# Kernel tuning notes

Measured on AMD Instinct MI355X. Metric: run time of the kernel, lower is better.

The kernel has to match this reference:

```python
import jax, jax.numpy as jnp
import numpy as np
import math

D_HEAD = 64
EPS = 1e-6


def _rms_norm(x, scale, eps):
    # compute in float32 like the torch reference (promote_types with float32)
    xf = x.astype(jnp.float32)
    ms = jnp.mean(xf * xf, axis=-1, keepdims=True)
    return (xf * (scale.astype(jnp.float32) * jax.lax.rsqrt(ms + eps))).astype(x.dtype)


def _apply_rotary(x, cos, sin):
    # rotate first 2*cos_dim channels, pass the rest through
    ro = cos.shape[-1] * 2
    xr, xp = x[..., :ro], x[..., ro:]
    c = jnp.concatenate([cos, cos], axis=-1)
    s = jnp.concatenate([sin, sin], axis=-1)
    x1, x2 = jnp.split(xr, 2, axis=-1)
    rot = jnp.concatenate([-x2, x1], axis=-1)
    return jnp.concatenate([xr * c + rot * s, xp], axis=-1)


def _nb_idx(L, k):
    # NATTEN neighborhood start: window of size k clamped inside [0, L)
    i = jnp.arange(L)
    start = jnp.clip(i - k // 2, 0, L - k)
    return start[:, None] + jnp.arange(k)[None, :]  # [L, k]


def setup_inputs() -> dict:
    key = jax.random.key(0)
    ks = jax.random.split(key, 6)
    n, H, W, d_model, cond_features = 2, 48, 48, 256, 256
    x = jax.random.normal(ks[0], (n, H, W, d_model), dtype=jnp.float32)
    axis = jnp.linspace(-1.0, 1.0, H, dtype=jnp.float32)
    gh, gw = jnp.meshgrid(axis, axis, indexing='ij')
    pos = jnp.stack([gh, gw], axis=-1)  # [H, W, 2]
    cond = jax.random.normal(ks[1], (n, cond_features), dtype=jnp.float32)
    w_norm = jax.random.normal(ks[2], (d_model, cond_features), dtype=jnp.float32) * 0.01
    w_qkv = jax.random.normal(ks[3], (3 * d_model, d_model), dtype=jnp.float32) / math.sqrt(d_model)
    w_out = jax.random.normal(ks[4], (d_model, d_model), dtype=jnp.float32) * 0.02
    return {"x": x, "pos": pos, "cond": cond, "w_norm": w_norm, "w_qkv": w_qkv,
            "w_out": w_out, "kernel_size": 7}


def reference(x, pos, cond, w_norm, w_qkv, w_out, kernel_size):
    n, H, W, d_model = x.shape
    e = D_HEAD
    nh = d_model // e
    k = kernel_size
    skip = x

    # AdaRMSNorm: scale = linear(cond) + 1, broadcast over h, w
    scale = (cond @ w_norm.T)[:, None, None, :] + 1.0  # [n,1,1,d_model]
    xn = _rms_norm(x, scale, EPS)

    # QKV projection -> [3, n, nh, H, W, e]
    qkv = (xn @ w_qkv.T).reshape(n, H, W, 3, nh, e)
    qkv = jnp.transpose(qkv, (3, 0, 4, 1, 2, 5))
    q, kk, v = qkv[0], qkv[1], qkv[2]

    # Axial RoPE: freqs buffer of AxialRoPE(d_head // 2)
    dim = e // 2
    nf = dim // 4
    freqs = jnp.exp(jnp.linspace(math.log(math.pi), math.log(10.0 * math.pi), nf + 1)[:-1]).astype(jnp.float32)
    fh = pos[..., 0:1] * freqs  # [H,W,nf]
    fw = pos[..., 1:2] * freqs
    fr = jnp.concatenate([fh, fw], axis=-1)  # [H,W,2*nf] == [H,W,e//4]
    cos, sin = jnp.cos(fr), jnp.sin(fr)
    q = _apply_rotary(q, cos, sin)
    kk = _apply_rotary(kk, cos, sin)
    q = q / math.sqrt(e)

    # 2D neighborhood attention (natten2dqk / natten2dav, dilation 1)
    idx_h = _nb_idx(H, k)  # [H,k]
    idx_w = _nb_idx(W, k)  # [W,k]
    kg = kk[:, :, idx_h][:, :, :, :, idx_w]  # [n,nh,H,k,W,k,e]
    vg = v[:, :, idx_h][:, :, :, :, idx_w]   # [n,nh,H,k,W,k,e]
    qk = jnp.einsum('bmije,bmipjqe->bmijpq', q, kg).reshape(n, nh, H, W, k * k)
    a = jax.nn.softmax(qk, axis=-1).reshape(n, nh, H, W, k, k)
    o = jnp.einsum('bmijpq,bmipjqe->bmije', a, vg)  # [n,nh,H,W,e]

    o = jnp.transpose(o, (0, 2, 3, 1, 4)).reshape(n, H, W, d_model)
    return o @ w_out.T + skip
```

## Files before the change

kernel.cpp:

```cpp
#include <hip/hip_runtime.h>
#include <math.h>

#define N_B 2
#define HH 48
#define WW 48
#define DM 256
#define NH 4
#define EH 64
#define KS 7
#define NPIX (N_B*HH*WW)

typedef _Float16 half8 __attribute__((ext_vector_type(8)));
typedef float float4v __attribute__((ext_vector_type(4)));

__global__ void scale_kernel(const float* __restrict__ cond,
                             const float* __restrict__ w_norm,
                             float* __restrict__ scale) {
    int b = blockIdx.x;
    int t = threadIdx.x, wave = t >> 6, lane = t & 63;
    int d = blockIdx.y*32 + wave*8 + (lane >> 3);
    int l8 = lane & 7;
    const float4* wr4 = (const float4*)(w_norm + (size_t)d*DM) + l8*8;
    const float4* c4  = (const float4*)(cond + (size_t)b*DM) + l8*8;
    float acc = 0.f;
    #pragma unroll
    for (int j = 0; j < 8; ++j) {
        float4 w = wr4[j], c = c4[j];
        acc += w.x*c.x + w.y*c.y + w.z*c.z + w.w*c.w;
    }
    acc += __shfl_xor(acc, 1, 64);
    acc += __shfl_xor(acc, 2, 64);
    acc += __shfl_xor(acc, 4, 64);
    if (l8 == 0) scale[b*DM + d] = acc + 1.0f;
}

__global__ void rmsnorm_kernel(const float* __restrict__ x,
                               const float* __restrict__ scale,
                               _Float16* __restrict__ xn) {
    int pix = blockIdx.x, t = threadIdx.x;
    int b = pix / (HH*WW);
    float v = x[(size_t)pix*DM + t];
    float ss = v*v;
    #pragma unroll
    for (int off = 32; off > 0; off >>= 1) ss += __shfl_xor(ss, off, 64);
    __shared__ float wsum[4];
    if ((t & 63) == 0) wsum[t>>6] = ss;
    __syncthreads();
    float tot = wsum[0]+wsum[1]+wsum[2]+wsum[3];
    float r = rsqrtf(tot*(1.0f/DM) + 1e-6f);
    xn[(size_t)pix*DM + t] = (_Float16)(v * scale[b*DM + t] * r);
}

__global__ __launch_bounds__(256) void gemm_qkv_f16(const _Float16* __restrict__ A,
                                                    const float* __restrict__ B,
                                                    const float* __restrict__ pos,
                                                    _Float16* __restrict__ qh,
                                                    _Float16* __restrict__ kh,
                                                    _Float16* __restrict__ vh) {
    const int K = DM, LDT = 40;
    __shared__ _Float16 As[64*LDT];
    __shared__ _Float16 Bs[64*LDT];
    int t = threadIdx.x;
    int wave = t >> 6, lane = t & 63;
    int m0 = blockIdx.x*64, n0 = blockIdx.y*64;
    int lr = t >> 2, lk = (t & 3) * 8;

    float4v acc[4];
    #pragma unroll
    for (int ni = 0; ni < 4; ++ni) acc[ni] = (float4v){0.f,0.f,0.f,0.f};

    int frow = lane & 15, kq = (lane >> 4) * 8;

    for (int k0 = 0; k0 < K; k0 += 32) {
        half8 a0 = *(const half8*)(A + (size_t)(m0 + lr)*K + k0 + lk);
        const float* bp = B + (size_t)(n0 + lr)*K + k0 + lk;
        float4 b0 = *(const float4*)bp;
        float4 b1 = *(const float4*)(bp + 4);
        half8 hb;
        hb[0]=(_Float16)b0.x; hb[1]=(_Float16)b0.y; hb[2]=(_Float16)b0.z; hb[3]=(_Float16)b0.w;
        hb[4]=(_Float16)b1.x; hb[5]=(_Float16)b1.y; hb[6]=(_Float16)b1.z; hb[7]=(_Float16)b1.w;
        __syncthreads();
        *(half8*)&As[lr*LDT + lk] = a0;
        *(half8*)&Bs[lr*LDT + lk] = hb;
        __syncthreads();
        half8 af = *(const half8*)&As[(wave*16 + frow)*LDT + kq];
        #pragma unroll
        for (int ni = 0; ni < 4; ++ni) {
            half8 bf = *(const half8*)&Bs[(ni*16 + frow)*LDT + kq];
            acc[ni] = __builtin_amdgcn_mfma_f32_16x16x32_f16(af, bf, acc[ni], 0, 0, 0);
        }
    }

    int sel  = n0 >> 8;
    int head = (n0 >> 6) & 3;
    _Float16* outp = (sel == 0) ? qh : (sel == 1) ? kh : vh;
    int col = lane & 15, rbase = (lane >> 4) * 4;
    float freq = __expf(1.14472988585f + (float)(col & 7) * 0.287823136624f);
    #pragma unroll
    for (int r = 0; r < 4; ++r) {
        int pix = m0 + wave*16 + rbase + r;
        float v0 = acc[0][r], v1 = acc[1][r], v2 = acc[2][r], v3 = acc[3][r];
        if (sel < 2) {
            int hw = pix % (HH*WW);
            float p = (col < 8) ? pos[hw*2] : pos[hw*2+1];
            float sn, cs;
            __sincosf(p*freq, &sn, &cs);
            float o0 = v0*cs - v1*sn;
            float o1 = v1*cs + v0*sn;
            v0 = o0; v1 = o1;
            if (sel == 0) { v0*=0.125f; v1*=0.125f; v2*=0.125f; v3*=0.125f; }
        }
        size_t base = (size_t)pix*DM + head*EH;
        outp[base +  0 + col] = (_Float16)v0;
        outp[base + 16 + col] = (_Float16)v1;
        outp[base + 32 + col] = (_Float16)v2;
        outp[base + 48 + col] = (_Float16)v3;
    }
}

__global__ __launch_bounds__(256) void attn_mfma(const _Float16* __restrict__ qg,
                                                 const _Float16* __restrict__ kg,
                                                 const _Float16* __restrict__ vg,
                                                 _Float16* __restrict__ obuf) {
    __shared__ _Float16 VT[64*232];
    __shared__ _Float16 SP[64*232];
    int t = threadIdx.x;
    int wave = t >> 6, lane = t & 63;
    int col = lane & 15, quad = lane >> 4;
    int ty = blockIdx.x / 6, tx = blockIdx.x % 6;
    int b = blockIdx.y >> 2, head = blockIdx.y & 3;
    int qh0 = ty*8, qw0 = tx*8;
    int rh0 = min(max(qh0-3, 0), HH-14);
    int rw0 = min(max(qw0-3, 0), WW-14);

    {
        int nbl = t & 31;
        int e0  = (t >> 5) * 8;
        #pragma unroll
        for (int pass = 0; pass < 7; ++pass) {
            int nb = pass*32 + nbl;
            int nr = nb >> 4, nc = nb & 15;
            int pix = (b*HH + rh0+nr)*WW + rw0 + nc;
            half8 vv = *(const half8*)(vg + (size_t)pix*DM + head*EH + e0);
            #pragma unroll
            for (int i = 0; i < 8; ++i)
                VT[(e0+i)*232 + nb] = vv[i];
        }
    }

    int qidx_a = wave*16 + col;
    int pixq = (b*HH + qh0 + (qidx_a>>3))*WW + qw0 + (qidx_a & 7);
    const _Float16* qp = qg + (size_t)pixq*DM + head*EH;
    half8 qf0 = *(const half8*)(qp + quad*8);
    half8 qf1 = *(const half8*)(qp + 32 + quad*8);

    float4v s[14];
    #pragma unroll
    for (int nr = 0; nr < 14; ++nr) {
        int pixk = (b*HH + rh0+nr)*WW + rw0 + col;
        const _Float16* kp = kg + (size_t)pixk*DM + head*EH;
        half8 kf0 = *(const half8*)(kp + quad*8);
        half8 kf1 = *(const half8*)(kp + 32 + quad*8);
        float4v a = (float4v){0.f,0.f,0.f,0.f};
        a = __builtin_amdgcn_mfma_f32_16x16x32_f16(qf0, kf0, a, 0, 0, 0);
        a = __builtin_amdgcn_mfma_f32_16x16x32_f16(qf1, kf1, a, 0, 0, 0);
        s[nr] = a;
    }

    int sh_[4], uw_[4];
    #pragma unroll
    for (int r = 0; r < 4; ++r) {
        int qidx = wave*16 + quad*4 + r;
        int qhh = qh0 + (qidx>>3), qww = qw0 + (qidx & 7);
        sh_[r] = min(max(qhh-3, 0), HH-KS);
        int sw_ = min(max(qww-3, 0), WW-KS);
        uw_[r] = rw0 + col - sw_;
    }
    #pragma unroll
    for (int nr = 0; nr < 14; ++nr)
        #pragma unroll
        for (int r = 0; r < 4; ++r) {
            int uh = rh0 + nr - sh_[r];
            bool ok = ((unsigned)uh < 7u) && ((unsigned)uw_[r] < 7u);
            s[nr][r] = ok ? s[nr][r] : -1e30f;
        }
    #pragma unroll
    for (int r = 0; r < 4; ++r) {
        float m = s[0][r];
        #pragma unroll
        for (int nr = 1; nr < 14; ++nr) m = fmaxf(m, s[nr][r]);
        m = fmaxf(m, __shfl_xor(m, 1, 64));
        m = fmaxf(m, __shfl_xor(m, 2, 64));
        m = fmaxf(m, __shfl_xor(m, 4, 64));
        m = fmaxf(m, __shfl_xor(m, 8, 64));
        float sum = 0.f;
        #pragma unroll
        for (int nr = 0; nr < 14; ++nr) { float p = __expf(s[nr][r] - m); s[nr][r] = p; sum += p; }
        sum += __shfl_xor(sum, 1, 64);
        sum += __shfl_xor(sum, 2, 64);
        sum += __shfl_xor(sum, 4, 64);
        sum += __shfl_xor(sum, 8, 64);
        float rs = 1.f / sum;
        #pragma unroll
        for (int nr = 0; nr < 14; ++nr)
            SP[(wave*16 + quad*4 + r)*232 + nr*16 + col] = (_Float16)(s[nr][r] * rs);
    }
    __syncthreads();

    float4v o[4];
    #pragma unroll
    for (int dt = 0; dt < 4; ++dt) o[dt] = (float4v){0.f,0.f,0.f,0.f};
    #pragma unroll
    for (int ks = 0; ks < 7; ++ks) {
        half8 pa = *(const half8*)&SP[(wave*16 + col)*232 + ks*32 + quad*8];
        #pragma unroll
        for (int dt = 0; dt < 4; ++dt) {
            half8 vf = *(const half8*)&VT[(dt*16 + col)*232 + ks*32 + quad*8];
            o[dt] = __builtin_amdgcn_mfma_f32_16x16x32_f16(pa, vf, o[dt], 0, 0, 0);
        }
    }
    #pragma unroll
    for (int r = 0; r < 4; ++r) {
        int qidx = wave*16 + quad*4 + r;
        int pix = (b*HH + qh0 + (qidx>>3))*WW + qw0 + (qidx & 7);
        #pragma unroll
        for (int dt = 0; dt < 4; ++dt)
            obuf[(size_t)pix*DM + head*EH + dt*16 + col] = (_Float16)o[dt][r];
    }
}

__global__ __launch_bounds__(256) void gemm_out_f16(const _Float16* __restrict__ A,
                                                    const float* __restrict__ B,
                                                    float* __restrict__ C,
                                                    const float* __restrict__ skip) {
    const int K = DM, N = DM, LDT = 40;
    __shared__ _Float16 As[64*LDT];
    __shared__ _Float16 Bs[64*LDT];
    int t = threadIdx.x;
    int wave = t >> 6, lane = t & 63;
    int m0 = blockIdx.x*64, n0 = blockIdx.y*64;
    int lr = t >> 2, lk = (t & 3) * 8;

    float4v acc[4];
    #pragma unroll
    for (int ni = 0; ni < 4; ++ni) acc[ni] = (float4v){0.f,0.f,0.f,0.f};

    int frow = lane & 15, kq = (lane >> 4) * 8;

    for (int k0 = 0; k0 < K; k0 += 32) {
        half8 a0 = *(const half8*)(A + (size_t)(m0 + lr)*K + k0 + lk);
        const float* bp = B + (size_t)(n0 + lr)*K + k0 + lk;
        float4 b0 = *(const float4*)bp;
        float4 b1 = *(const float4*)(bp + 4);
        half8 hb;
        hb[0]=(_Float16)b0.x; hb[1]=(_Float16)b0.y; hb[2]=(_Float16)b0.z; hb[3]=(_Float16)b0.w;
        hb[4]=(_Float16)b1.x; hb[5]=(_Float16)b1.y; hb[6]=(_Float16)b1.z; hb[7]=(_Float16)b1.w;
        __syncthreads();
        *(half8*)&As[lr*LDT + lk] = a0;
        *(half8*)&Bs[lr*LDT + lk] = hb;
        __syncthreads();
        half8 af = *(const half8*)&As[(wave*16 + frow)*LDT + kq];
        #pragma unroll
        for (int ni = 0; ni < 4; ++ni) {
            half8 bf = *(const half8*)&Bs[(ni*16 + frow)*LDT + kq];
            acc[ni] = __builtin_amdgcn_mfma_f32_16x16x32_f16(af, bf, acc[ni], 0, 0, 0);
        }
    }

    int col = lane & 15, rbase = (lane >> 4) * 4;
    #pragma unroll
    for (int ni = 0; ni < 4; ++ni) {
        #pragma unroll
        for (int r = 0; r < 4; ++r) {
            int row = m0 + wave*16 + rbase + r;
            int c   = n0 + ni*16 + col;
            C[(size_t)row*N + c] = acc[ni][r] + skip[(size_t)row*N + c];
        }
    }
}

extern "C" void kernel_launch(void* const* d_in, const int* in_sizes, int n_in,
                              void* d_out, int out_size, void* d_ws, size_t ws_size,
                              hipStream_t stream) {
    const float* x      = (const float*)d_in[0];
    const float* pos    = (const float*)d_in[1];
    const float* cond   = (const float*)d_in[2];
    const float* w_norm = (const float*)d_in[3];
    const float* w_qkv  = (const float*)d_in[4];
    const float* w_out  = (const float*)d_in[5];
    float* out = (float*)d_out;
    char* base = (char*)d_ws;

    const size_t SZH = (size_t)NPIX*DM*2;
    const size_t PAD = 4096;
    float*    scale  = (float*)(base);
    _Float16* xn_h   = (_Float16*)(base + PAD);
    _Float16* qh     = (_Float16*)(base + PAD + 1*(SZH+PAD));
    _Float16* kh     = (_Float16*)(base + PAD + 2*(SZH+PAD));
    _Float16* vh     = (_Float16*)(base + PAD + 3*(SZH+PAD));
    _Float16* obuf_h = (_Float16*)(base + PAD + 4*(SZH+PAD));

    scale_kernel<<<dim3(N_B, 8), 256, 0, stream>>>(cond, w_norm, scale);
    rmsnorm_kernel<<<dim3(NPIX), dim3(DM), 0, stream>>>(x, scale, xn_h);
    gemm_qkv_f16<<<dim3(NPIX/64, 12), 256, 0, stream>>>(xn_h, w_qkv, pos, qh, kh, vh);
    attn_mfma<<<dim3(36, N_B*NH), 256, 0, stream>>>(qh, kh, vh, obuf_h);
    gemm_out_f16<<<dim3(NPIX/64, DM/64), 256, 0, stream>>>(obuf_h, w_out, out, x);
}
```

Before: 105.8 us.

## Fuse RMSNorm into QKV GEMM, stage full-K tiles, shrink output GEMM tile

Drops the separate RMSNorm kernel. Each QKV GEMM block now loads its 64 rows of x in fp32, computes the per-row RMS with shuffles, applies scale and converts to fp16 straight into shared memory. Both GEMMs now stage the entire K=256 tile once instead of looping over 32-wide slices with two barriers per step. The output GEMM uses 32-row tiles to double the block count. The cost is much larger LDS use per block (about 66KB for QKV), which may lower occupancy. The normalization is also recomputed by each of the 12 column blocks, so x is reread 12 times.

```diff
diff --git a/kernel.cpp b/kernel.cpp
--- a/kernel.cpp
+++ b/kernel.cpp
@@ -34,59 +34,73 @@
     if (l8 == 0) scale[b*DM + d] = acc + 1.0f;
 }
 
-__global__ void rmsnorm_kernel(const float* __restrict__ x,
-                               const float* __restrict__ scale,
-                               _Float16* __restrict__ xn) {
-    int pix = blockIdx.x, t = threadIdx.x;
-    int b = pix / (HH*WW);
-    float v = x[(size_t)pix*DM + t];
-    float ss = v*v;
-    #pragma unroll
-    for (int off = 32; off > 0; off >>= 1) ss += __shfl_xor(ss, off, 64);
-    __shared__ float wsum[4];
-    if ((t & 63) == 0) wsum[t>>6] = ss;
-    __syncthreads();
-    float tot = wsum[0]+wsum[1]+wsum[2]+wsum[3];
-    float r = rsqrtf(tot*(1.0f/DM) + 1e-6f);
-    xn[(size_t)pix*DM + t] = (_Float16)(v * scale[b*DM + t] * r);
-}
-
-__global__ __launch_bounds__(256) void gemm_qkv_f16(const _Float16* __restrict__ A,
-                                                    const float* __restrict__ B,
-                                                    const float* __restrict__ pos,
-                                                    _Float16* __restrict__ qh,
-                                                    _Float16* __restrict__ kh,
-                                                    _Float16* __restrict__ vh) {
-    const int K = DM, LDT = 40;
-    __shared__ _Float16 As[64*LDT];
-    __shared__ _Float16 Bs[64*LDT];
+__global__ __launch_bounds__(256) void fused_qkv(const float* __restrict__ x,
+                                                 const float* __restrict__ scale,
+                                                 const float* __restrict__ B,
+                                                 const float* __restrict__ pos,
+                                                 _Float16* __restrict__ qh,
+                                                 _Float16* __restrict__ kh,
+                                                 _Float16* __restrict__ vh) {
+    const int K = DM, LDA = 264;
+    __shared__ _Float16 As[64*LDA];
+    __shared__ _Float16 Bs[64*LDA];
+    __shared__ float scale_sh[DM];
     int t = threadIdx.x;
     int wave = t >> 6, lane = t & 63;
     int m0 = blockIdx.x*64, n0 = blockIdx.y*64;
-    int lr = t >> 2, lk = (t & 3) * 8;
-
+    int b = m0 / (HH*WW);
+
+    scale_sh[t] = scale[b*DM + t];
+
+    int row = t >> 2, seg = t & 3;
+    const float4* xp = (const float4*)(x + (size_t)(m0+row)*DM + seg*64);
+    float4 xr[16];
+    float ss = 0.f;
+    #pragma unroll
+    for (int j = 0; j < 16; ++j) {
+        xr[j] = xp[j];
+        ss += xr[j].x*xr[j].x + xr[j].y*xr[j].y + xr[j].z*xr[j].z + xr[j].w*xr[j].w;
+    }
+    ss += __shfl_xor(ss, 1, 64);
+    ss += __shfl_xor(ss, 2, 64);
+    float rms = rsqrtf(ss*(1.0f/DM) + 1e-6f);
+    __syncthreads();
+
+    #pragma unroll
+    for (int j = 0; j < 8; ++j) {
+        int ch = seg*64 + j*8;
+        float4 a = xr[2*j], c = xr[2*j+1];
+        half8 hv;
+        hv[0]=(_Float16)(a.x*scale_sh[ch+0]*rms); hv[1]=(_Float16)(a.y*scale_sh[ch+1]*rms);
+        hv[2]=(_Float16)(a.z*scale_sh[ch+2]*rms); hv[3]=(_Float16)(a.w*scale_sh[ch+3]*rms);
+        hv[4]=(_Float16)(c.x*scale_sh[ch+4]*rms); hv[5]=(_Float16)(c.y*scale_sh[ch+5]*rms);
+        hv[6]=(_Float16)(c.z*scale_sh[ch+6]*rms); hv[7]=(_Float16)(c.w*scale_sh[ch+7]*rms);
+        *(half8*)&As[row*LDA + ch] = hv;
+    }
+    {
+        const float4* bp = (const float4*)(B + (size_t)(n0+row)*K + seg*64);
+        #pragma unroll
+        for (int j = 0; j < 8; ++j) {
+            float4 b0 = bp[2*j], b1 = bp[2*j+1];
+            half8 hb;
+            hb[0]=(_Float16)b0.x; hb[1]=(_Float16)b0.y; hb[2]=(_Float16)b0.z; hb[3]=(_Float16)b0.w;
+            hb[4]=(_Float16)b1.x; hb[5]=(_Float16)b1.y; hb[6]=(_Float16)b1.z; hb[7]=(_Float16)b1.w;
+            *(half8*)&Bs[row*LDA + seg*64 + j*8] = hb;
+        }
+    }
+    __syncthreads();
+
+    int frow = lane & 15, kq = (lane >> 4) * 8;
     float4v acc[4];
     #pragma unroll
     for (int ni = 0; ni < 4; ++ni) acc[ni] = (float4v){0.f,0.f,0.f,0.f};
-
-    int frow = lane & 15, kq = (lane >> 4) * 8;
-
-    for (int k0 = 0; k0 < K; k0 += 32) {
-        half8 a0 = *(const half8*)(A + (size_t)(m0 + lr)*K + k0 + lk);
-        const float* bp = B + (size_t)(n0 + lr)*K + k0 + lk;
-        float4 b0 = *(const float4*)bp;
-        float4 b1 = *(const float4*)(bp + 4);
-        half8 hb;
-        hb[0]=(_Float16)b0.x; hb[1]=(_Float16)b0.y; hb[2]=(_Float16)b0.z; hb[3]=(_Float16)b0.w;
-        hb[4]=(_Float16)b1.x; hb[5]=(_Float16)b1.y; hb[6]=(_Float16)b1.z; hb[7]=(_Float16)b1.w;
-        __syncthreads();
-        *(half8*)&As[lr*LDT + lk] = a0;
-        *(half8*)&Bs[lr*LDT + lk] = hb;
-        __syncthreads();
-        half8 af = *(const half8*)&As[(wave*16 + frow)*LDT + kq];
+    #pragma unroll
+    for (int ks = 0; ks < 8; ++ks) {
+        int k0 = ks*32;
+        half8 af = *(const half8*)&As[(wave*16 + frow)*LDA + k0 + kq];
         #pragma unroll
         for (int ni = 0; ni < 4; ++ni) {
-            half8 bf = *(const half8*)&Bs[(ni*16 + frow)*LDT + kq];
+            half8 bf = *(const half8*)&Bs[(ni*16 + frow)*LDA + k0 + kq];
             acc[ni] = __builtin_amdgcn_mfma_f32_16x16x32_f16(af, bf, acc[ni], 0, 0, 0);
         }
     }
@@ -233,48 +247,59 @@
                                                     const float* __restrict__ B,
                                                     float* __restrict__ C,
                                                     const float* __restrict__ skip) {
-    const int K = DM, N = DM, LDT = 40;
-    __shared__ _Float16 As[64*LDT];
-    __shared__ _Float16 Bs[64*LDT];
+    const int K = DM, N = DM, LDA = 264;
+    __shared__ _Float16 As[32*LDA];
+    __shared__ _Float16 Bs[64*LDA];
     int t = threadIdx.x;
     int wave = t >> 6, lane = t & 63;
-    int m0 = blockIdx.x*64, n0 = blockIdx.y*64;
-    int lr = t >> 2, lk = (t & 3) * 8;
-
-    float4v acc[4];
-    #pragma unroll
-    for (int ni = 0; ni < 4; ++ni) acc[ni] = (float4v){0.f,0.f,0.f,0.f};
+    int m0 = blockIdx.x*32, n0 = blockIdx.y*64;
+
+    {
+        int row = t >> 3, seg = t & 7;
+        const _Float16* ap = A + (size_t)(m0+row)*K + seg*32;
+        #pragma unroll
+        for (int j = 0; j < 4; ++j)
+            *(half8*)&As[row*LDA + seg*32 + j*8] = *(const half8*)(ap + j*8);
+    }
+    {
+        int row = t >> 2, seg = t & 3;
+        const float4* bp = (const float4*)(B + (size_t)(n0+row)*K + seg*64);
+        #pragma unroll
+        for (int j = 0; j < 8; ++j) {
+            float4 b0 = bp[2*j], b1 = bp[2*j+1];
+            half8 hb;
+            hb[0]=(_Float16)b0.x; hb[1]=(_Float16)b0.y; hb[2]=(_Float16)b0.z; hb[3]=(_Float16)b0.w;
+            hb[4]=(_Float16)b1.x; hb[5]=(_Float16)b1.y; hb[6]=(_Float16)b1.z; hb[7]=(_Float16)b1.w;
+            *(half8*)&Bs[row*LDA + seg*64 + j*8] = hb;
+        }
+    }
+    __syncthreads();
 
     int frow = lane & 15, kq = (lane >> 4) * 8;
-
-    for (int k0 = 0; k0 < K; k0 += 32) {
-        half8 a0 = *(const half8*)(A + (size_t)(m0 + lr)*K + k0 + lk);
-        const float* bp = B + (size_t)(n0 + lr)*K + k0 + lk;
-        float4 b0 = *(const float4*)bp;
-        float4 b1 = *(const float4*)(bp + 4);
-        half8 hb;
-        hb[0]=(_Float16)b0.x; hb[1]=(_Float16)b0.y; hb[2]=(_Float16)b0.z; hb[3]=(_Float16)b0.w;
-        hb[4]=(_Float16)b1.x; hb[5]=(_Float16)b1.y; hb[6]=(_Float16)b1.z; hb[7]=(_Float16)b1.w;
-        __syncthreads();
-        *(half8*)&As[lr*LDT + lk] = a0;
-        *(half8*)&Bs[lr*LDT + lk] = hb;
-        __syncthreads();
-        half8 af = *(const half8*)&As[(wave*16 + frow)*LDT + kq];
-        #pragma unroll
-        for (int ni = 0; ni < 4; ++ni) {
-            half8 bf = *(const half8*)&Bs[(ni*16 + frow)*LDT + kq];
+    int mrow  = (wave & 1) * 16;
+    int nbase = (wave >> 1) * 32;
+    float4v acc[2];
+    acc[0] = (float4v){0.f,0.f,0.f,0.f};
+    acc[1] = (float4v){0.f,0.f,0.f,0.f};
+    #pragma unroll
+    for (int ks = 0; ks < 8; ++ks) {
+        int k0 = ks*32;
+        half8 af = *(const half8*)&As[(mrow + frow)*LDA + k0 + kq];
+        #pragma unroll
+        for (int ni = 0; ni < 2; ++ni) {
+            half8 bf = *(const half8*)&Bs[(nbase + ni*16 + frow)*LDA + k0 + kq];
             acc[ni] = __builtin_amdgcn_mfma_f32_16x16x32_f16(af, bf, acc[ni], 0, 0, 0);
         }
     }
 
     int col = lane & 15, rbase = (lane >> 4) * 4;
     #pragma unroll
-    for (int ni = 0; ni < 4; ++ni) {
+    for (int ni = 0; ni < 2; ++ni) {
         #pragma unroll
         for (int r = 0; r < 4; ++r) {
-            int row = m0 + wave*16 + rbase + r;
-            int c   = n0 + ni*16 + col;
-            C[(size_t)row*N + c] = acc[ni][r] + skip[(size_t)row*N + c];
+            int rowg = m0 + mrow + rbase + r;
+            int c    = n0 + nbase + ni*16 + col;
+            C[(size_t)rowg*N + c] = acc[ni][r] + skip[(size_t)rowg*N + c];
         }
     }
 }
@@ -294,15 +319,13 @@
     const size_t SZH = (size_t)NPIX*DM*2;
     const size_t PAD = 4096;
     float*    scale  = (float*)(base);
-    _Float16* xn_h   = (_Float16*)(base + PAD);
-    _Float16* qh     = (_Float16*)(base + PAD + 1*(SZH+PAD));
-    _Float16* kh     = (_Float16*)(base + PAD + 2*(SZH+PAD));
-    _Float16* vh     = (_Float16*)(base + PAD + 3*(SZH+PAD));
-    _Float16* obuf_h = (_Float16*)(base + PAD + 4*(SZH+PAD));
+    _Float16* qh     = (_Float16*)(base + PAD + 0*(SZH+PAD));
+    _Float16* kh     = (_Float16*)(base + PAD + 1*(SZH+PAD));
+    _Float16* vh     = (_Float16*)(base + PAD + 2*(SZH+PAD));
+    _Float16* obuf_h = (_Float16*)(base + PAD + 3*(SZH+PAD));
 
     scale_kernel<<<dim3(N_B, 8), 256, 0, stream>>>(cond, w_norm, scale);
-    rmsnorm_kernel<<<dim3(NPIX), dim3(DM), 0, stream>>>(x, scale, xn_h);
-    gemm_qkv_f16<<<dim3(NPIX/64, 12), 256, 0, stream>>>(xn_h, w_qkv, pos, qh, kh, vh);
+    fused_qkv<<<dim3(NPIX/64, 12), 256, 0, stream>>>(x, scale, w_qkv, pos, qh, kh, vh);
     attn_mfma<<<dim3(36, N_B*NH), 256, 0, stream>>>(qh, kh, vh, obuf_h);
-    gemm_out_f16<<<dim3(NPIX/64, DM/64), 256, 0, stream>>>(obuf_h, w_out, out, x);
-}
+    gemm_out_f16<<<dim3(NPIX/32, DM/64), 256, 0, stream>>>(obuf_h, w_out, out, x);
+}
```

Result: slower. 116.1 us (+9.8%).

## Fuse all five kernels into one persistent megakernel with grid barriers

Applied to the files above, without the earlier changes.

Replaces the five separate launches (scale, rmsnorm, QKV GEMM, neighborhood attention, output GEMM) with a single persistent kernel of 512 blocks. Each stage runs as a grid-stride loop over its tiles, and stages are separated by atomic-counter grid barriers. The intent is to remove per-launch overhead and inter-kernel gaps. In exchange it adds a memset launch, spin-wait barrier costs, and a deadlock risk if all 512 blocks cannot be co-resident. The attention stage has only 288 tiles, so many blocks sit idle there.

```diff
diff --git a/kernel.cpp b/kernel.cpp
--- a/kernel.cpp
+++ b/kernel.cpp
@@ -9,272 +9,287 @@
 #define EH 64
 #define KS 7
 #define NPIX (N_B*HH*WW)
+#define GRID 512
 
 typedef _Float16 half8 __attribute__((ext_vector_type(8)));
 typedef float float4v __attribute__((ext_vector_type(4)));
 
-__global__ void scale_kernel(const float* __restrict__ cond,
-                             const float* __restrict__ w_norm,
-                             float* __restrict__ scale) {
-    int b = blockIdx.x;
-    int t = threadIdx.x, wave = t >> 6, lane = t & 63;
-    int d = blockIdx.y*32 + wave*8 + (lane >> 3);
-    int l8 = lane & 7;
-    const float4* wr4 = (const float4*)(w_norm + (size_t)d*DM) + l8*8;
-    const float4* c4  = (const float4*)(cond + (size_t)b*DM) + l8*8;
-    float acc = 0.f;
-    #pragma unroll
-    for (int j = 0; j < 8; ++j) {
-        float4 w = wr4[j], c = c4[j];
-        acc += w.x*c.x + w.y*c.y + w.z*c.z + w.w*c.w;
-    }
-    acc += __shfl_xor(acc, 1, 64);
-    acc += __shfl_xor(acc, 2, 64);
-    acc += __shfl_xor(acc, 4, 64);
-    if (l8 == 0) scale[b*DM + d] = acc + 1.0f;
-}
-
-__global__ void rmsnorm_kernel(const float* __restrict__ x,
-                               const float* __restrict__ scale,
-                               _Float16* __restrict__ xn) {
-    int pix = blockIdx.x, t = threadIdx.x;
-    int b = pix / (HH*WW);
-    float v = x[(size_t)pix*DM + t];
-    float ss = v*v;
-    #pragma unroll
-    for (int off = 32; off > 0; off >>= 1) ss += __shfl_xor(ss, off, 64);
-    __shared__ float wsum[4];
-    if ((t & 63) == 0) wsum[t>>6] = ss;
-    __syncthreads();
-    float tot = wsum[0]+wsum[1]+wsum[2]+wsum[3];
-    float r = rsqrtf(tot*(1.0f/DM) + 1e-6f);
-    xn[(size_t)pix*DM + t] = (_Float16)(v * scale[b*DM + t] * r);
-}
-
-__global__ __launch_bounds__(256) void gemm_qkv_f16(const _Float16* __restrict__ A,
-                                                    const float* __restrict__ B,
-                                                    const float* __restrict__ pos,
-                                                    _Float16* __restrict__ qh,
-                                                    _Float16* __restrict__ kh,
-                                                    _Float16* __restrict__ vh) {
-    const int K = DM, LDT = 40;
-    __shared__ _Float16 As[64*LDT];
-    __shared__ _Float16 Bs[64*LDT];
+#define GBAR(idx) do { \
+    __syncthreads(); \
+    if (t == 0) { \
+        __threadfence(); \
+        __hip_atomic_fetch_add(&cnt[idx], 1, __ATOMIC_RELEASE, __HIP_MEMORY_SCOPE_AGENT); \
+        while (__hip_atomic_load(&cnt[idx], __ATOMIC_ACQUIRE, __HIP_MEMORY_SCOPE_AGENT) < (int)gridDim.x) \
+            __builtin_amdgcn_s_sleep(1); \
+        __threadfence(); \
+    } \
+    __syncthreads(); \
+} while (0)
+
+__global__ __launch_bounds__(256, 2) void mega(const float* __restrict__ x,
+                                               const float* __restrict__ pos,
+                                               const float* __restrict__ cond,
+                                               const float* __restrict__ w_norm,
+                                               const float* __restrict__ w_qkv,
+                                               const float* __restrict__ w_out,
+                                               float* __restrict__ out,
+                                               int* __restrict__ cnt,
+                                               float* __restrict__ scale,
+                                               _Float16* __restrict__ xn,
+                                               _Float16* __restrict__ qh,
+                                               _Float16* __restrict__ kh,
+                                               _Float16* __restrict__ vh,
+                                               _Float16* __restrict__ obuf) {
+    int bid = blockIdx.x, nblk = gridDim.x;
     int t = threadIdx.x;
     int wave = t >> 6, lane = t & 63;
-    int m0 = blockIdx.x*64, n0 = blockIdx.y*64;
-    int lr = t >> 2, lk = (t & 3) * 8;
-
-    float4v acc[4];
-    #pragma unroll
-    for (int ni = 0; ni < 4; ++ni) acc[ni] = (float4v){0.f,0.f,0.f,0.f};
-
-    int frow = lane & 15, kq = (lane >> 4) * 8;
-
-    for (int k0 = 0; k0 < K; k0 += 32) {
-        half8 a0 = *(const half8*)(A + (size_t)(m0 + lr)*K + k0 + lk);
-        const float* bp = B + (size_t)(n0 + lr)*K + k0 + lk;
-        float4 b0 = *(const float4*)bp;
-        float4 b1 = *(const float4*)(bp + 4);
-        half8 hb;
-        hb[0]=(_Float16)b0.x; hb[1]=(_Float16)b0.y; hb[2]=(_Float16)b0.z; hb[3]=(_Float16)b0.w;
-        hb[4]=(_Float16)b1.x; hb[5]=(_Float16)b1.y; hb[6]=(_Float16)b1.z; hb[7]=(_Float16)b1.w;
+
+    __shared__ union {
+        struct { _Float16 As[64*40]; _Float16 Bs[64*40]; } g;
+        struct { _Float16 VT[64*232]; _Float16 SP[64*232]; } at;
+        float wsum[4];
+    } sm;
+
+    if (bid < 16) {
+        int b = bid & 1, yg = bid >> 1;
+        int d = yg*32 + wave*8 + (lane >> 3);
+        int l8 = lane & 7;
+        const float4* wr4 = (const float4*)(w_norm + (size_t)d*DM) + l8*8;
+        const float4* c4  = (const float4*)(cond + (size_t)b*DM) + l8*8;
+        float acc = 0.f;
+        #pragma unroll
+        for (int j = 0; j < 8; ++j) {
+            float4 w = wr4[j], c = c4[j];
+            acc += w.x*c.x + w.y*c.y + w.z*c.z + w.w*c.w;
+        }
+        acc += __shfl_xor(acc, 1, 64);
+        acc += __shfl_xor(acc, 2, 64);
+        acc += __shfl_xor(acc, 4, 64);
+        if (l8 == 0) scale[b*DM + d] = acc + 1.0f;
+    }
+    GBAR(0);
+
+    for (int pix = bid; pix < NPIX; pix += nblk) {
+        int b = pix / (HH*WW);
+        float v = x[(size_t)pix*DM + t];
+        float ss = v*v;
+        #pragma unroll
+        for (int off = 32; off > 0; off >>= 1) ss += __shfl_xor(ss, off, 64);
+        if ((t & 63) == 0) sm.wsum[t>>6] = ss;
         __syncthreads();
-        *(half8*)&As[lr*LDT + lk] = a0;
-        *(half8*)&Bs[lr*LDT + lk] = hb;
+        float tot = sm.wsum[0]+sm.wsum[1]+sm.wsum[2]+sm.wsum[3];
+        float r = rsqrtf(tot*(1.0f/DM) + 1e-6f);
+        xn[(size_t)pix*DM + t] = (_Float16)(v * scale[b*DM + t] * r);
         __syncthreads();
-        half8 af = *(const half8*)&As[(wave*16 + frow)*LDT + kq];
-        #pragma unroll
-        for (int ni = 0; ni < 4; ++ni) {
-            half8 bf = *(const half8*)&Bs[(ni*16 + frow)*LDT + kq];
-            acc[ni] = __builtin_amdgcn_mfma_f32_16x16x32_f16(af, bf, acc[ni], 0, 0, 0);
+    }
+    GBAR(1);
+
+    {
+        const int K = DM, LDT = 40;
+        int lr = t >> 2, lk = (t & 3) * 8;
+        int frow = lane & 15, kq = (lane >> 4) * 8;
+        int col = lane & 15, rbase = (lane >> 4) * 4;
+        float freq = __expf(1.14472988585f + (float)(col & 7) * 0.287823136624f);
+        for (int tile = bid; tile < 72*12; tile += nblk) {
+            int m0 = (tile % 72)*64, n0 = (tile / 72)*64;
+            float4v acc[4];
+            #pragma unroll
+            for (int ni = 0; ni < 4; ++ni) acc[ni] = (float4v){0.f,0.f,0.f,0.f};
+            for (int k0 = 0; k0 < K; k0 += 32) {
+                half8 a0 = *(const half8*)(xn + (size_t)(m0 + lr)*K + k0 + lk);
+                const float* bp = w_qkv + (size_t)(n0 + lr)*K + k0 + lk;
+                float4 b0 = *(const float4*)bp;
+                float4 b1 = *(const float4*)(bp + 4);
+                half8 hb;
+                hb[0]=(_Float16)b0.x; hb[1]=(_Float16)b0.y; hb[2]=(_Float16)b0.z; hb[3]=(_Float16)b0.w;
+                hb[4]=(_Float16)b1.x; hb[5]=(_Float16)b1.y; hb[6]=(_Float16)b1.z; hb[7]=(_Float16)b1.w;
+                __syncthreads();
+                *(half8*)&sm.g.As[lr*LDT + lk] = a0;
+                *(half8*)&sm.g.Bs[lr*LDT + lk] = hb;
+                __syncthreads();
+                half8 af = *(const half8*)&sm.g.As[(wave*16 + frow)*LDT + kq];
+                #pragma unroll
+                for (int ni = 0; ni < 4; ++ni) {
+                    half8 bf = *(const half8*)&sm.g.Bs[(ni*16 + frow)*LDT + kq];
+                    acc[ni] = __builtin_amdgcn_mfma_f32_16x16x32_f16(af, bf, acc[ni], 0, 0, 0);
+                }
+            }
+            int sel  = n0 >> 8;
+            int head = (n0 >> 6) & 3;
+            _Float16* outp = (sel == 0) ? qh : (sel == 1) ? kh : vh;
+            #pragma unroll
+            for (int r = 0; r < 4; ++r) {
+                int pix = m0 + wave*16 + rbase + r;
+                float v0 = acc[0][r], v1 = acc[1][r], v2 = acc[2][r], v3 = acc[3][r];
+                if (sel < 2) {
+                    int hw = pix % (HH*WW);
+                    float p = (col < 8) ? pos[hw*2] : pos[hw*2+1];
+                    float sn, cs;
+                    __sincosf(p*freq, &sn, &cs);
+                    float o0 = v0*cs - v1*sn;
+                    float o1 = v1*cs + v0*sn;
+                    v0 = o0; v1 = o1;
+                    if (sel == 0) { v0*=0.125f; v1*=0.125f; v2*=0.125f; v3*=0.125f; }
+                }
+                size_t base = (size_t)pix*DM + head*EH;
+                outp[base +  0 + col] = (_Float16)v0;
+                outp[base + 16 + col] = (_Float16)v1;
+                outp[base + 32 + col] = (_Float16)v2;
+                outp[base + 48 + col] = (_Float16)v3;
+            }
+            __syncthreads();
         }
     }
-
-    int sel  = n0 >> 8;
-    int head = (n0 >> 6) & 3;
-    _Float16* outp = (sel == 0) ? qh : (sel == 1) ? kh : vh;
-    int col = lane & 15, rbase = (lane >> 4) * 4;
-    float freq = __expf(1.14472988585f + (float)(col & 7) * 0.287823136624f);
-    #pragma unroll
-    for (int r = 0; r < 4; ++r) {
-        int pix = m0 + wave*16 + rbase + r;
-        float v0 = acc[0][r], v1 = acc[1][r], v2 = acc[2][r], v3 = acc[3][r];
-        if (sel < 2) {
-            int hw = pix % (HH*WW);
-            float p = (col < 8) ? pos[hw*2] : pos[hw*2+1];
-            float sn, cs;
-            __sincosf(p*freq, &sn, &cs);
-            float o0 = v0*cs - v1*sn;
-            float o1 = v1*cs + v0*sn;
-            v0 = o0; v1 = o1;
-            if (sel == 0) { v0*=0.125f; v1*=0.125f; v2*=0.125f; v3*=0.125f; }
+    GBAR(2);
+
+    {
+        int col = lane & 15, quad = lane >> 4;
+        for (int tile = bid; tile < 36*N_B*NH; tile += nblk) {
+            int bx = tile % 36, by = tile / 36;
+            int ty = bx / 6, tx = bx % 6;
+            int b = by >> 2, head = by & 3;
+            int qh0 = ty*8, qw0 = tx*8;
+            int rh0 = min(max(qh0-3, 0), HH-14);
+            int rw0 = min(max(qw0-3, 0), WW-14);
+
+            {
+                int nbl = t & 31;
+                int e0  = (t >> 5) * 8;
+                #pragma unroll
+                for (int pass = 0; pass < 7; ++pass) {
+                    int nb = pass*32 + nbl;
+                    int nr = nb >> 4, nc = nb & 15;
+                    int pix = (b*HH + rh0+nr)*WW + rw0 + nc;
+                    half8 vv = *(const half8*)(vh + (size_t)pix*DM + head*EH + e0);
+                    #pragma unroll
+                    for (int i = 0; i < 8; ++i)
+                        sm.at.VT[(e0+i)*232 + nb] = vv[i];
+                }
+            }
+
+            int qidx_a = wave*16 + col;
+            int pixq = (b*HH + qh0 + (qidx_a>>3))*WW + qw0 + (qidx_a & 7);
+            const _Float16* qp = qh + (size_t)pixq*DM + head*EH;
+            half8 qf0 = *(const half8*)(qp + quad*8);
+            half8 qf1 = *(const half8*)(qp + 32 + quad*8);
+
+            float4v s[14];
+            #pragma unroll
+            for (int nr = 0; nr < 14; ++nr) {
+                int pixk = (b*HH + rh0+nr)*WW + rw0 + col;
+                const _Float16* kp = kh + (size_t)pixk*DM + head*EH;
+                half8 kf0 = *(const half8*)(kp + quad*8);
+                half8 kf1 = *(const half8*)(kp + 32 + quad*8);
+                float4v a = (float4v){0.f,0.f,0.f,0.f};
+                a = __builtin_amdgcn_mfma_f32_16x16x32_f16(qf0, kf0, a, 0, 0, 0);
+                a = __builtin_amdgcn_mfma_f32_16x16x32_f16(qf1, kf1, a, 0, 0, 0);
+                s[nr] = a;
+            }
+
+            int sh_[4], uw_[4];
+            #pragma unroll
+            for (int r = 0; r < 4; ++r) {
+                int qidx = wave*16 + quad*4 + r;
+                int qhh = qh0 + (qidx>>3), qww = qw0 + (qidx & 7);
+                sh_[r] = min(max(qhh-3, 0), HH-KS);
+                int sw_ = min(max(qww-3, 0), WW-KS);
+                uw_[r] = rw0 + col - sw_;
+            }
+            #pragma unroll
+            for (int nr = 0; nr < 14; ++nr)
+                #pragma unroll
+                for (int r = 0; r < 4; ++r) {
+                    int uh = rh0 + nr - sh_[r];
+                    bool ok = ((unsigned)uh < 7u) && ((unsigned)uw_[r] < 7u);
+                    s[nr][r] = ok ? s[nr][r] : -1e30f;
+                }
+            #pragma unroll
+            for (int r = 0; r < 4; ++r) {
+                float m = s[0][r];
+                #pragma unroll
+                for (int nr = 1; nr < 14; ++nr) m = fmaxf(m, s[nr][r]);
+                m = fmaxf(m, __shfl_xor(m, 1, 64));
+                m = fmaxf(m, __shfl_xor(m, 2, 64));
+                m = fmaxf(m, __shfl_xor(m, 4, 64));
+                m = fmaxf(m, __shfl_xor(m, 8, 64));
+                float sum = 0.f;
+                #pragma unroll
+                for (int nr = 0; nr < 14; ++nr) { float p = __expf(s[nr][r] - m); s[nr][r] = p; sum += p; }
+                sum += __shfl_xor(sum, 1, 64);
+                sum += __shfl_xor(sum, 2, 64);
+                sum += __shfl_xor(sum, 4, 64);
+                sum += __shfl_xor(sum, 8, 64);
+                float rs = 1.f / sum;
+                #pragma unroll
+                for (int nr = 0; nr < 14; ++nr)
+                    sm.at.SP[(wave*16 + quad*4 + r)*232 + nr*16 + col] = (_Float16)(s[nr][r] * rs);
+            }
+            __syncthreads();
+
+            float4v o[4];
+            #pragma unroll
+            for (int dt = 0; dt < 4; ++dt) o[dt] = (float4v){0.f,0.f,0.f,0.f};
+            #pragma unroll
+            for (int ks = 0; ks < 7; ++ks) {
+                half8 pa = *(const half8*)&sm.at.SP[(wave*16 + col)*232 + ks*32 + quad*8];
+                #pragma unroll
+                for (int dt = 0; dt < 4; ++dt) {
+                    half8 vf = *(const half8*)&sm.at.VT[(dt*16 + col)*232 + ks*32 + quad*8];
+                    o[dt] = __builtin_amdgcn_mfma_f32_16x16x32_f16(pa, vf, o[dt], 0, 0, 0);
+                }
+            }
+            #pragma unroll
+            for (int r = 0; r < 4; ++r) {
+                int qidx = wave*16 + quad*4 + r;
+                int pix = (b*HH + qh0 + (qidx>>3))*WW + qw0 + (qidx & 7);
+                #pragma unroll
+                for (int dt = 0; dt < 4; ++dt)
+                    obuf[(size_t)pix*DM + head*EH + dt*16 + col] = (_Float16)o[dt][r];
+            }
+            __syncthreads();
         }
-        size_t base = (size_t)pix*DM + head*EH;
-        outp[base +  0 + col] = (_Float16)v0;
-        outp[base + 16 + col] = (_Float16)v1;
-        outp[base + 32 + col] = (_Float16)v2;
-        outp[base + 48 + col] = (_Float16)v3;
-    }
-}
-
-__global__ __launch_bounds__(256) void attn_mfma(const _Float16* __restrict__ qg,
-                                                 const _Float16* __restrict__ kg,
-                                                 const _Float16* __restrict__ vg,
-                                                 _Float16* __restrict__ obuf) {
-    __shared__ _Float16 VT[64*232];
-    __shared__ _Float16 SP[64*232];
-    int t = threadIdx.x;
-    int wave = t >> 6, lane = t & 63;
-    int col = lane & 15, quad = lane >> 4;
-    int ty = blockIdx.x / 6, tx = blockIdx.x % 6;
-    int b = blockIdx.y >> 2, head = blockIdx.y & 3;
-    int qh0 = ty*8, qw0 = tx*8;
-    int rh0 = min(max(qh0-3, 0), HH-14);
-    int rw0 = min(max(qw0-3, 0), WW-14);
+    }
+    GBAR(3);
 
     {
-        int nbl = t & 31;
-        int e0  = (t >> 5) * 8;
-        #pragma unroll
-        for (int pass = 0; pass < 7; ++pass) {
-            int nb = pass*32 + nbl;
-            int nr = nb >> 4, nc = nb & 15;
-            int pix = (b*HH + rh0+nr)*WW + rw0 + nc;
-            half8 vv = *(const half8*)(vg + (size_t)pix*DM + head*EH + e0);
-            #pragma unroll
-            for (int i = 0; i < 8; ++i)
-                VT[(e0+i)*232 + nb] = vv[i];
-        }
-    }
-
-    int qidx_a = wave*16 + col;
-    int pixq = (b*HH + qh0 + (qidx_a>>3))*WW + qw0 + (qidx_a & 7);
-    const _Float16* qp = qg + (size_t)pixq*DM + head*EH;
-    half8 qf0 = *(const half8*)(qp + quad*8);
-    half8 qf1 = *(const half8*)(qp + 32 + quad*8);
-
-    float4v s[14];
-    #pragma unroll
-    for (int nr = 0; nr < 14; ++nr) {
-        int pixk = (b*HH + rh0+nr)*WW + rw0 + col;
-        const _Float16* kp = kg + (size_t)pixk*DM + head*EH;
-        half8 kf0 = *(const half8*)(kp + quad*8);
-        half8 kf1 = *(const half8*)(kp + 32 + quad*8);
-        float4v a = (float4v){0.f,0.f,0.f,0.f};
-        a = __builtin_amdgcn_mfma_f32_16x16x32_f16(qf0, kf0, a, 0, 0, 0);
-        a = __builtin_amdgcn_mfma_f32_16x16x32_f16(qf1, kf1, a, 0, 0, 0);
-        s[nr] = a;
-    }
-
-    int sh_[4], uw_[4];
-    #pragma unroll
-    for (int r = 0; r < 4; ++r) {
-        int qidx = wave*16 + quad*4 + r;
-        int qhh = qh0 + (qidx>>3), qww = qw0 + (qidx & 7);
-        sh_[r] = min(max(qhh-3, 0), HH-KS);
-        int sw_ = min(max(qww-3, 0), WW-KS);
-        uw_[r] = rw0 + col - sw_;
-    }
-    #pragma unroll
-    for (int nr = 0; nr < 14; ++nr)
-        #pragma unroll
-        for (int r = 0; r < 4; ++r) {
-            int uh = rh0 + nr - sh_[r];
-            bool ok = ((unsigned)uh < 7u) && ((unsigned)uw_[r] < 7u);
-            s[nr][r] = ok ? s[nr][r] : -1e30f;
-        }
-    #pragma unroll
-    for (int r = 0; r < 4; ++r) {
-        float m = s[0][r];
-        #pragma unroll
-        for (int nr = 1; nr < 14; ++nr) m = fmaxf(m, s[nr][r]);
-        m = fmaxf(m, __shfl_xor(m, 1, 64));
-        m = fmaxf(m, __shfl_xor(m, 2, 64));
-        m = fmaxf(m, __shfl_xor(m, 4, 64));
-        m = fmaxf(m, __shfl_xor(m, 8, 64));
-        float sum = 0.f;
-        #pragma unroll
-        for (int nr = 0; nr < 14; ++nr) { float p = __expf(s[nr][r] - m); s[nr][r] = p; sum += p; }
-        sum += __shfl_xor(sum, 1, 64);
-        sum += __shfl_xor(sum, 2, 64);
-        sum += __shfl_xor(sum, 4, 64);
-        sum += __shfl_xor(sum, 8, 64);
-        float rs = 1.f / sum;
-        #pragma unroll
-        for (int nr = 0; nr < 14; ++nr)
-            SP[(wave*16 + quad*4 + r)*232 + nr*16 + col] = (_Float16)(s[nr][r] * rs);
-    }
-    __syncthreads();
-
-    float4v o[4];
-    #pragma unroll
-    for (int dt = 0; dt < 4; ++dt) o[dt] = (float4v){0.f,0.f,0.f,0.f};
-    #pragma unroll
-    for (int ks = 0; ks < 7; ++ks) {
-        half8 pa = *(const half8*)&SP[(wave*16 + col)*232 + ks*32 + quad*8];
-        #pragma unroll
-        for (int dt = 0; dt < 4; ++dt) {
-            half8 vf = *(const half8*)&VT[(dt*16 + col)*232 + ks*32 + quad*8];
-            o[dt] = __builtin_amdgcn_mfma_f32_16x16x32_f16(pa, vf, o[dt], 0, 0, 0);
-        }
-    }
-    #pragma unroll
-    for (int r = 0; r < 4; ++r) {
-        int qidx = wave*16 + quad*4 + r;
-        int pix = (b*HH + qh0 + (qidx>>3))*WW + qw0 + (qidx & 7);
-        #pragma unroll
-        for (int dt = 0; dt < 4; ++dt)
-            obuf[(size_t)pix*DM + head*EH + dt*16 + col] = (_Float16)o[dt][r];
-    }
-}
-
-__global__ __launch_bounds__(256) void gemm_out_f16(const _Float16* __restrict__ A,
-                                                    const float* __restrict__ B,
-                                                    float* __restrict__ C,
-                                                    const float* __restrict__ skip) {
-    const int K = DM, N = DM, LDT = 40;
-    __shared__ _Float16 As[64*LDT];
-    __shared__ _Float16 Bs[64*LDT];
-    int t = threadIdx.x;
-    int wave = t >> 6, lane = t & 63;
-    int m0 = blockIdx.x*64, n0 = blockIdx.y*64;
-    int lr = t >> 2, lk = (t & 3) * 8;
-
-    float4v acc[4];
-    #pragma unroll
-    for (int ni = 0; ni < 4; ++ni) acc[ni] = (float4v){0.f,0.f,0.f,0.f};
-
-    int frow = lane & 15, kq = (lane >> 4) * 8;
-
-    for (int k0 = 0; k0 < K; k0 += 32) {
-        half8 a0 = *(const half8*)(A + (size_t)(m0 + lr)*K + k0 + lk);
-        const float* bp = B + (size_t)(n0 + lr)*K + k0 + lk;
-        float4 b0 = *(const float4*)bp;
-        float4 b1 = *(const float4*)(bp + 4);
-        half8 hb;
-        hb[0]=(_Float16)b0.x; hb[1]=(_Float16)b0.y; hb[2]=(_Float16)b0.z; hb[3]=(_Float16)b0.w;
-        hb[4]=(_Float16)b1.x; hb[5]=(_Float16)b1.y; hb[6]=(_Float16)b1.z; hb[7]=(_Float16)b1.w;
-        __syncthreads();
-        *(half8*)&As[lr*LDT + lk] = a0;
-        *(half8*)&Bs[lr*LDT + lk] = hb;
-        __syncthreads();
-        half8 af = *(const half8*)&As[(wave*16 + frow)*LDT + kq];
-        #pragma unroll
-        for (int ni = 0; ni < 4; ++ni) {
-            half8 bf = *(const half8*)&Bs[(ni*16 + frow)*LDT + kq];
-            acc[ni] = __builtin_amdgcn_mfma_f32_16x16x32_f16(af, bf, acc[ni], 0, 0, 0);
-        }
-    }
-
-    int col = lane & 15, rbase = (lane >> 4) * 4;
-    #pragma unroll
-    for (int ni = 0; ni < 4; ++ni) {
-        #pragma unroll
-        for (int r = 0; r < 4; ++r) {
-            int row = m0 + wave*16 + rbase + r;
-            int c   = n0 + ni*16 + col;
-            C[(size_t)row*N + c] = acc[ni][r] + skip[(size_t)row*N + c];
+        const int K = DM, N = DM, LDT = 40;
+        int lr = t >> 2, lk = (t & 3) * 8;
+        int frow = lane & 15, kq = (lane >> 4) * 8;
+        int col = lane & 15, rbase = (lane >> 4) * 4;
+        for (int tile = bid; tile < 72*4; tile += nblk) {
+            int m0 = (tile % 72)*64, n0 = (tile / 72)*64;
+            float4v acc[4];
+            #pragma unroll
+            for (int ni = 0; ni < 4; ++ni) acc[ni] = (float4v){0.f,0.f,0.f,0.f};
+            for (int k0 = 0; k0 < K; k0 += 32) {
+                half8 a0 = *(const half8*)(obuf + (size_t)(m0 + lr)*K + k0 + lk);
+                const float* bp = w_out + (size_t)(n0 + lr)*K + k0 + lk;
+                float4 b0 = *(const float4*)bp;
+                float4 b1 = *(const float4*)(bp + 4);
+                half8 hb;
+                hb[0]=(_Float16)b0.x; hb[1]=(_Float16)b0.y; hb[2]=(_Float16)b0.z; hb[3]=(_Float16)b0.w;
+                hb[4]=(_Float16)b1.x; hb[5]=(_Float16)b1.y; hb[6]=(_Float16)b1.z; hb[7]=(_Float16)b1.w;
+                __syncthreads();
+                *(half8*)&sm.g.As[lr*LDT + lk] = a0;
+                *(half8*)&sm.g.Bs[lr*LDT + lk] = hb;
+                __syncthreads();
+                half8 af = *(const half8*)&sm.g.As[(wave*16 + frow)*LDT + kq];
+                #pragma unroll
+                for (int ni = 0; ni < 4; ++ni) {
+                    half8 bf = *(const half8*)&sm.g.Bs[(ni*16 + frow)*LDT + kq];
+                    acc[ni] = __builtin_amdgcn_mfma_f32_16x16x32_f16(af, bf, acc[ni], 0, 0, 0);
+                }
+            }
+            #pragma unroll
+            for (int ni = 0; ni < 4; ++ni) {
+                #pragma unroll
+                for (int r = 0; r < 4; ++r) {
+                    int rowg = m0 + wave*16 + rbase + r;
+                    int c    = n0 + ni*16 + col;
+                    out[(size_t)rowg*N + c] = acc[ni][r] + x[(size_t)rowg*N + c];
+                }
+            }
+            __syncthreads();
         }
     }
 }
@@ -293,16 +308,15 @@
 
     const size_t SZH = (size_t)NPIX*DM*2;
     const size_t PAD = 4096;
-    float*    scale  = (float*)(base);
-    _Float16* xn_h   = (_Float16*)(base + PAD);
+    int*      cnt    = (int*)base;
+    float*    scale  = (float*)(base + 256);
+    _Float16* xn_h   = (_Float16*)(base + PAD + 0*(SZH+PAD));
     _Float16* qh     = (_Float16*)(base + PAD + 1*(SZH+PAD));
     _Float16* kh     = (_Float16*)(base + PAD + 2*(SZH+PAD));
     _Float16* vh     = (_Float16*)(base + PAD + 3*(SZH+PAD));
     _Float16* obuf_h = (_Float16*)(base + PAD + 4*(SZH+PAD));
 
-    scale_kernel<<<dim3(N_B, 8), 256, 0, stream>>>(cond, w_norm, scale);
-    rmsnorm_kernel<<<dim3(NPIX), dim3(DM), 0, stream>>>(x, scale, xn_h);
-    gemm_qkv_f16<<<dim3(NPIX/64, 12), 256, 0, stream>>>(xn_h, w_qkv, pos, qh, kh, vh);
-    attn_mfma<<<dim3(36, N_B*NH), 256, 0, stream>>>(qh, kh, vh, obuf_h);
-    gemm_out_f16<<<dim3(NPIX/64, DM/64), 256, 0, stream>>>(obuf_h, w_out, out, x);
+    hipMemsetAsync(cnt, 0, 64, stream);
+    mega<<<dim3(GRID), dim3(256), 0, stream>>>(x, pos, cond, w_norm, w_qkv, w_out, out,
+                                               cnt, scale, xn_h, qh, kh, vh, obuf_h);
 }
```

New measurement: 410.4 us. 288% more time.
